# Kernel tuning notes

Hardware: AMD Instinct MI355X
Metric: run time of the kernel (lower is better)

The kernel has to match this reference:

```python
import jax, jax.numpy as jnp
import numpy as np

TOP_K = 2


def setup_inputs() -> dict:
    key = jax.random.key(0)
    k1, k2, k3, k4 = jax.random.split(key, 4)
    B, D, H, E = 16384, 1024, 1024, 8
    return {
        "x": jax.random.normal(k1, (B, D), dtype=jnp.float32),
        "Wv": jax.random.normal(k2, (E, D, H), dtype=jnp.float32),
        "Wg": jax.random.normal(k3, (E, D, H), dtype=jnp.float32),
        "gate_w": jax.random.normal(k4, (E, D), dtype=jnp.float32) * (1.0 / np.sqrt(D)),
        "gate_b": jnp.zeros((E,), dtype=jnp.float32),
    }


def reference(x, Wv, Wg, gate_w, gate_b):
    # Router: softmax over expert logits, then top-k selection.
    logits = x @ gate_w.T + gate_b                      # [B, E]
    probs = jax.nn.softmax(logits, axis=1)
    topk_scores, topk_idx = jax.lax.top_k(probs, TOP_K)  # [B, K]

    B, E = probs.shape
    # Scatter top-k scores into a dense [B, E] combine matrix (zeros elsewhere).
    combine = jnp.zeros((B, E), dtype=probs.dtype).at[
        jnp.arange(B)[:, None], topk_idx
    ].add(topk_scores)

    # Dense per-expert SwiGLU; combine matrix zeros out non-selected experts,
    # so the math matches the grouped-gemm top-k dispatch exactly.
    v = jnp.einsum("bd,edh->beh", x, Wv)                # [B, E, H]
    g = jnp.einsum("bd,edh->beh", x, Wg)                # [B, E, H]
    act = v * jax.nn.sigmoid(g)                         # SwiGLU-style gating
    return jnp.einsum("be,beh->bh", combine, act)       # weighted combine [B, H]
```

## Files before the change

kernel.cpp:

```cpp
#include <hip/hip_runtime.h>

#define D_DIM 1024
#define H_DIM 1024
#define E_NUM 8
#define BM 256
#define BN 256
#define BK 64
#define NT (D_DIM / BK)
#define CAP 5120
#define RT_TOK 32
#define RT_BLKS (16384 / RT_TOK)
#define TW_BLKS (16 * 16 * 2 * E_NUM)

typedef __attribute__((ext_vector_type(8))) _Float16 h8v;
typedef __attribute__((ext_vector_type(4))) float f4v;

__device__ __forceinline__ unsigned short f2h(float f) {
  union { _Float16 h; unsigned short u; } c;
  c.h = (_Float16)f;
  return c.u;
}

__device__ __forceinline__ void gl2lds16(const void* g, void* l) {
  __builtin_amdgcn_global_load_lds(
      (const __attribute__((address_space(1))) unsigned int*)g,
      (__attribute__((address_space(3))) unsigned int*)l, 16, 0, 0);
}

__device__ __forceinline__ unsigned ldsaddr(const void* p) {
  return (unsigned)(unsigned long long)(const __attribute__((address_space(3))) void*)p;
}

__global__ __launch_bounds__(256) void prep_kernel(
    const float4* __restrict__ x4, const float4* __restrict__ gw4,
    const float* __restrict__ gb, int* __restrict__ counts,
    int* __restrict__ bucket, float* __restrict__ scoreB,
    int* __restrict__ slotOf, ushort4* __restrict__ xh4,
    const float* __restrict__ Wv, const float* __restrict__ Wg,
    unsigned short* __restrict__ Wc) {
  __shared__ float4 gwS[E_NUM * 256];
  __shared__ float tile[64][65];
  __shared__ short eSelS[RT_TOK][2];
  __shared__ float sSelS[RT_TOK][2];
  __shared__ int lCnt[E_NUM], lBase[E_NUM];
  __shared__ unsigned char lOff[RT_TOK][2];
  int tid = threadIdx.x;
  int bid = blockIdx.x;

  if (bid >= RT_BLKS) {
    int fb = bid - RT_BLKS;
    int hx = fb & 15, dy = (fb >> 4) & 15, z = fb >> 8;
    const float* W = (z & 1) ? Wg : Wv;
    int mat = z & 1;
    int e = z >> 1;
    int h0 = hx * 64, d0 = dy * 64;
    const float* Wp = W + (size_t)e * D_DIM * H_DIM;
    unsigned short* Wcp = Wc + (size_t)e * (2 * H_DIM) * D_DIM;
#pragma unroll
    for (int j = 0; j < 4; j++) {
      int id = tid + 256 * j;
      int dd = id >> 4, hc = id & 15;
      float4 v = *(const float4*)(Wp + (size_t)(d0 + dd) * H_DIM + h0 + hc * 4);
      tile[dd][hc * 4 + 0] = v.x;
      tile[dd][hc * 4 + 1] = v.y;
      tile[dd][hc * 4 + 2] = v.z;
      tile[dd][hc * 4 + 3] = v.w;
    }
    __syncthreads();
#pragma unroll
    for (int j = 0; j < 2; j++) {
      int id = tid + 256 * j;
      int h_ = id >> 3, dc = id & 7;
      unsigned short tmp[8];
#pragma unroll
      for (int k = 0; k < 8; k++) tmp[k] = f2h(tile[dc * 8 + k][h_]);
      int hg = h0 + h_;
      int ng = ((hg >> 4) << 5) | (mat << 4) | (hg & 15);
      *(uint4*)(Wcp + (size_t)ng * D_DIM + d0 + dc * 8) = *(uint4*)tmp;
    }
    return;
  }

  for (int i = tid; i < E_NUM * 256; i += 256) gwS[i] = gw4[i];
  if (tid < E_NUM) lCnt[tid] = 0;
  __syncthreads();
  int wid = tid >> 6, lane = tid & 63;
  for (int rep = 0; rep < RT_TOK / 4; rep++) {
    int t = wid * (RT_TOK / 4) + rep;
    int b = bid * RT_TOK + t;
    float acc[E_NUM];
#pragma unroll
    for (int e = 0; e < E_NUM; e++) acc[e] = 0.0f;
#pragma unroll
    for (int i = 0; i < 4; i++) {
      float4 xv = x4[(size_t)b * 256 + i * 64 + lane];
      ushort4 o;
      o.x = f2h(xv.x); o.y = f2h(xv.y); o.z = f2h(xv.z); o.w = f2h(xv.w);
      xh4[(size_t)b * 256 + i * 64 + lane] = o;
#pragma unroll
      for (int e = 0; e < E_NUM; e++) {
        float4 w = gwS[e * 256 + i * 64 + lane];
        acc[e] += xv.x * w.x + xv.y * w.y + xv.z * w.z + xv.w * w.w;
      }
    }
#pragma unroll
    for (int e = 0; e < E_NUM; e++) {
#pragma unroll
      for (int off = 32; off > 0; off >>= 1) acc[e] += __shfl_down(acc[e], off);
    }
    if (lane == 0) {
      float l[E_NUM];
#pragma unroll
      for (int e = 0; e < E_NUM; e++) l[e] = acc[e] + gb[e];
      int i0 = 0;
#pragma unroll
      for (int e = 1; e < E_NUM; e++) if (l[e] > l[i0]) i0 = e;
      int i1 = (i0 == 0) ? 1 : 0;
#pragma unroll
      for (int e = 0; e < E_NUM; e++) if (e != i0 && l[e] > l[i1]) i1 = e;
      float mx = l[i0];
      float denom = 0.0f;
#pragma unroll
      for (int e = 0; e < E_NUM; e++) denom += __expf(l[e] - mx);
      eSelS[t][0] = (short)i0; sSelS[t][0] = 1.0f / denom;
      eSelS[t][1] = (short)i1; sSelS[t][1] = __expf(l[i1] - mx) / denom;
    }
  }
  __syncthreads();
  if (tid < RT_TOK) {
    lOff[tid][0] = (unsigned char)atomicAdd(&lCnt[eSelS[tid][0]], 1);
    lOff[tid][1] = (unsigned char)atomicAdd(&lCnt[eSelS[tid][1]], 1);
  }
  __syncthreads();
  if (tid < E_NUM) lBase[tid] = atomicAdd(&counts[tid * 32], lCnt[tid]);
  __syncthreads();
  if (tid < RT_TOK) {
    int b = bid * RT_TOK + tid;
#pragma unroll
    for (int j = 0; j < 2; j++) {
      int e = eSelS[tid][j];
      int pos = lBase[e] + lOff[tid][j];
      if (pos < CAP) {
        int slot = e * CAP + pos;
        bucket[slot] = b;
        scoreB[slot] = sSelS[tid][j];
        slotOf[b * 2 + j] = slot;
      }
    }
  }
}


#define DSR(dst, areg, IMM)                                                   \
  asm volatile("ds_read_b128 %0, %1 offset:%c2"                               \
               : "=v"(dst) : "v"(areg), "i"(IMM))

#define OFFS(CB, HI) ((CB) * 32768 + (HI) * 16384)

#define RD12_P0(CB) do {                                                      \
    DSR(bf[0][0], bB0, OFFS(CB, 0) + 0);                                      \
    DSR(bf[1][0], bB0, OFFS(CB, 0) + 2048);                                   \
    DSR(af[0][0], aA0, OFFS(CB, 0) + 0);                                      \
    DSR(af[1][0], aA0, OFFS(CB, 0) + 2048);                                   \
    DSR(af[2][0], aA0, OFFS(CB, 0) + 4096);                                   \
    DSR(af[3][0], aA0, OFFS(CB, 0) + 6144);                                   \
    DSR(bf[0][1], bB1, OFFS(CB, 0) + 0);                                      \
    DSR(bf[1][1], bB1, OFFS(CB, 0) + 2048);                                   \
    DSR(af[0][1], aA1, OFFS(CB, 0) + 0);                                      \
    DSR(af[1][1], aA1, OFFS(CB, 0) + 2048);                                   \
    DSR(af[2][1], aA1, OFFS(CB, 0) + 4096);                                   \
    DSR(af[3][1], aA1, OFFS(CB, 0) + 6144);                                   \
  } while (0)

#define RD8_A(CB, HI) do {                                                    \
    DSR(af[0][0], aA0, OFFS(CB, HI) + 0);                                     \
    DSR(af[1][0], aA0, OFFS(CB, HI) + 2048);                                  \
    DSR(af[2][0], aA0, OFFS(CB, HI) + 4096);                                  \
    DSR(af[3][0], aA0, OFFS(CB, HI) + 6144);                                  \
    DSR(af[0][1], aA1, OFFS(CB, HI) + 0);                                     \
    DSR(af[1][1], aA1, OFFS(CB, HI) + 2048);                                  \
    DSR(af[2][1], aA1, OFFS(CB, HI) + 4096);                                  \
    DSR(af[3][1], aA1, OFFS(CB, HI) + 6144);                                  \
  } while (0)

#define RD4_B(CB, HI) do {                                                    \
    DSR(bf[0][0], bB0, OFFS(CB, HI) + 0);                                     \
    DSR(bf[1][0], bB0, OFFS(CB, HI) + 2048);                                  \
    DSR(bf[0][1], bB1, OFFS(CB, HI) + 0);                                     \
    DSR(bf[1][1], bB1, OFFS(CB, HI) + 2048);                                  \
  } while (0)

#define MFMA_S(MO, NO, S)                                                     \
  {                                                                           \
    _Pragma("unroll") for (int m = 0; m < 4; m++) {                           \
      _Pragma("unroll") for (int n = 0; n < 2; n++) {                         \
        acc[(MO) + m][(NO) + n] = __builtin_amdgcn_mfma_f32_16x16x32_f16(     \
            af[m][S], bf[n][S], acc[(MO) + m][(NO) + n], 0, 0, 0);            \
      }                                                                       \
    }                                                                         \
  }

#define PH_BAR() __builtin_amdgcn_s_barrier()
#define LGKM(N) do {                                                          \
    asm volatile("s_waitcnt lgkmcnt(" #N ")" ::: "memory");                   \
    __builtin_amdgcn_sched_barrier(0);                                        \
  } while (0)
#define VMW(N) asm volatile("s_waitcnt vmcnt(" #N ")" ::: "memory")
#define PRIO1() __builtin_amdgcn_s_setprio(1)
#define PRIO0() __builtin_amdgcn_s_setprio(0)

#define TILE_N(CB) do {                                                       \
                           \
    RD12_P0(CB);                                                              \
    gl2lds16(pA[0], &As[(CB) ^ 1][0 * 4096 + dst0]);                          \
    gl2lds16(pA[1], &As[(CB) ^ 1][1 * 4096 + dst0]);                          \
    LGKM(6);  PRIO1(); MFMA_S(0, 0, 0); PRIO0();                              \
    LGKM(0);  PRIO1(); MFMA_S(0, 0, 1); PRIO0();                              \
    VMW(4); PH_BAR();                                                         \
                               \
    RD4_B(CB, 1);                                                             \
    gl2lds16(pB[0], &Bs[(CB) ^ 1][0 * 4096 + dst0]);                          \
    gl2lds16(pB[1], &Bs[(CB) ^ 1][1 * 4096 + dst0]);                          \
    LGKM(2);  PRIO1(); MFMA_S(0, 2, 0); PRIO0();                              \
    LGKM(0);  PRIO1(); MFMA_S(0, 2, 1); PRIO0();                              \
    VMW(4); PH_BAR();                                                         \
                   \
    RD8_A(CB, 1);                                                             \
    gl2lds16(pB[2], &Bs[(CB) ^ 1][2 * 4096 + dst0]);                          \
    gl2lds16(pB[3], &Bs[(CB) ^ 1][3 * 4096 + dst0]);                          \
    LGKM(4);  PRIO1(); MFMA_S(4, 2, 0); PRIO0();                              \
    LGKM(0);  PRIO1(); MFMA_S(4, 2, 1); PRIO0();                              \
                     \
    RD4_B(CB, 0);                                                             \
    gl2lds16(pA[2], &As[(CB) ^ 1][2 * 4096 + dst0]);                          \
    gl2lds16(pA[3], &As[(CB) ^ 1][3 * 4096 + dst0]);                          \
    LGKM(2);  PRIO1(); MFMA_S(4, 0, 0); PRIO0();                              \
    LGKM(0);  PRIO1(); MFMA_S(4, 0, 1); PRIO0();                              \
    VMW(4); PH_BAR();                                                         \
    _Pragma("unroll") for (int i = 0; i < 4; i++) { pA[i] += BK; pB[i] += BK; } \
  } while (0)

template <bool USE_PARTIAL>
__global__ __launch_bounds__(512, 2) void moe_gemm_kernel(
    const unsigned short* __restrict__ xh, const unsigned short* __restrict__ Wc,
    const int* __restrict__ counts, const int* __restrict__ bucket,
    const float* __restrict__ scoreB, _Float16* __restrict__ partial,
    float* __restrict__ out, int B) {
  int e = blockIdx.z;
  int cnt = counts[e * 32];
  int m0 = blockIdx.x * BM;
  if (m0 >= cnt) return;
  int n0 = blockIdx.y * BN;

  __shared__ unsigned short As[2][BM * BK];
  __shared__ unsigned short Bs[2][BN * BK];
  __shared__ int tokS[BM];
  __shared__ float scS[BM];

  int tid = threadIdx.x;
  if (tid < BM) {
    int gr = m0 + tid;
    bool vld = gr < cnt;
    tokS[tid] = vld ? bucket[e * CAP + gr] : 0;
    scS[tid] = vld ? scoreB[e * CAP + gr] : 0.0f;
  }
  __syncthreads();

  int wid = tid >> 6, lane = tid & 63;
  int wm = wid & 1, wn = wid >> 1;
  int quad = lane >> 4, lr = lane & 15;

  int rA = tid >> 3;
  int ksw = ((tid & 7) ^ (rA & 7)) * 8;
  const unsigned short* WcE = Wc + (size_t)e * (2 * H_DIM) * D_DIM;
  const unsigned short* pA[4];
  const unsigned short* pB[4];
#pragma unroll
  for (int i = 0; i < 4; i++) {
    pA[i] = xh + (size_t)tokS[i * 64 + rA] * D_DIM + ksw;
    pB[i] = WcE + (size_t)(n0 + i * 64 + rA) * D_DIM + ksw;
  }
  int dst0 = tid * 8;

  unsigned swz0 = (unsigned)(((0 * 4 + quad) ^ (lr & 7)) * 16);
  unsigned swz1 = (unsigned)(((1 * 4 + quad) ^ (lr & 7)) * 16);
  unsigned ldsA = ldsaddr(&As[0][0]);
  unsigned ldsB = ldsaddr(&Bs[0][0]);
  unsigned aA0 = ldsA + (unsigned)(wm * 8192 + lr * 128) + swz0;
  unsigned aA1 = ldsA + (unsigned)(wm * 8192 + lr * 128) + swz1;
  unsigned bB0 = ldsB + (unsigned)(wn * 4096 + lr * 128) + swz0;
  unsigned bB1 = ldsB + (unsigned)(wn * 4096 + lr * 128) + swz1;

  f4v acc[8][4];
#pragma unroll
  for (int m = 0; m < 8; m++)
#pragma unroll
    for (int n = 0; n < 4; n++) acc[m][n] = (f4v){0.f, 0.f, 0.f, 0.f};

  gl2lds16(pA[0], &As[0][0 * 4096 + dst0]);
  gl2lds16(pA[1], &As[0][1 * 4096 + dst0]);
  gl2lds16(pB[0], &Bs[0][0 * 4096 + dst0]);
  gl2lds16(pB[1], &Bs[0][1 * 4096 + dst0]);
  gl2lds16(pB[2], &Bs[0][2 * 4096 + dst0]);
  gl2lds16(pB[3], &Bs[0][3 * 4096 + dst0]);
  gl2lds16(pA[2], &As[0][2 * 4096 + dst0]);
  gl2lds16(pA[3], &As[0][3 * 4096 + dst0]);
#pragma unroll
  for (int i = 0; i < 4; i++) { pA[i] += BK; pB[i] += BK; }
  VMW(4);
  PH_BAR();

  h8v af[4][2], bf[2][2];

  for (int it = 0; it < 7; ++it) {
    TILE_N(0);
    TILE_N(1);
  }
  TILE_N(0);

  {
    RD12_P0(1);
    LGKM(6);  PRIO1(); MFMA_S(0, 0, 0); PRIO0();
    LGKM(0);  PRIO1(); MFMA_S(0, 0, 1); PRIO0();
    VMW(2); PH_BAR();
    RD4_B(1, 1);
    LGKM(2);  PRIO1(); MFMA_S(0, 2, 0); PRIO0();
    LGKM(0);  PRIO1(); MFMA_S(0, 2, 1); PRIO0();
    VMW(0); PH_BAR();
    RD8_A(1, 1);
    LGKM(4);  PRIO1(); MFMA_S(4, 2, 0); PRIO0();
    LGKM(0);  PRIO1(); MFMA_S(4, 2, 1); PRIO0();
    RD4_B(1, 0);
    LGKM(2);  PRIO1(); MFMA_S(4, 0, 0); PRIO0();
    LGKM(0);  PRIO1(); MFMA_S(4, 0, 1); PRIO0();
  }

  int hb = blockIdx.y * 128 + wn * 16 + lr;
#pragma unroll
  for (int m = 0; m < 8; m++) {
    int rb = ((m < 4) ? (wm * 64 + m * 16) : (128 + wm * 64 + (m - 4) * 16)) + quad * 4;
#pragma unroll
    for (int r = 0; r < 4; r++) {
      int rr = rb + r;
      float sc = scS[rr];
      if (USE_PARTIAL) {
        _Float16* pr = partial + (size_t)(e * CAP + m0 + rr) * H_DIM;
#pragma unroll
        for (int p = 0; p < 2; p++) {
          float v = acc[m][2 * p][r];
          float g = acc[m][2 * p + 1][r];
          pr[hb + p * 64] = (_Float16)(v * sc / (1.0f + __expf(-g)));
        }
      } else {
        int tok = tokS[rr];
#pragma unroll
        for (int p = 0; p < 2; p++) {
          float v = acc[m][2 * p][r];
          float g = acc[m][2 * p + 1][r];
          atomicAdd(&out[(size_t)tok * H_DIM + hb + p * 64],
                    v * sc / (1.0f + __expf(-g)));
        }
      }
    }
  }
}

__global__ __launch_bounds__(256) void gather_kernel(
    const _Float16* __restrict__ partial, const int* __restrict__ slotOf,
    float* __restrict__ out) {
  int b = blockIdx.x * 2 + (threadIdx.x >> 7);
  int t = threadIdx.x & 127;
  int s0 = slotOf[b * 2], s1 = slotOf[b * 2 + 1];
  if ((unsigned)s0 >= E_NUM * CAP) s0 = 0;
  if ((unsigned)s1 >= E_NUM * CAP) s1 = 0;
  h8v a = ((const h8v*)(partial + (size_t)s0 * H_DIM))[t];
  h8v c = ((const h8v*)(partial + (size_t)s1 * H_DIM))[t];
  float4 o0, o1;
  o0.x = (float)a[0] + (float)c[0];
  o0.y = (float)a[1] + (float)c[1];
  o0.z = (float)a[2] + (float)c[2];
  o0.w = (float)a[3] + (float)c[3];
  o1.x = (float)a[4] + (float)c[4];
  o1.y = (float)a[5] + (float)c[5];
  o1.z = (float)a[6] + (float)c[6];
  o1.w = (float)a[7] + (float)c[7];
  float4* op = (float4*)(out + (size_t)b * H_DIM);
  op[t * 2] = o0;
  op[t * 2 + 1] = o1;
}

extern "C" void kernel_launch(void* const* d_in, const int* in_sizes, int n_in,
                              void* d_out, int out_size, void* d_ws, size_t ws_size,
                              hipStream_t stream) {
  const float* x = (const float*)d_in[0];
  const float* Wv = (const float*)d_in[1];
  const float* Wg = (const float*)d_in[2];
  const float* gw = (const float*)d_in[3];
  const float* gb = (const float*)d_in[4];
  float* out = (float*)d_out;
  const int B = in_sizes[0] / D_DIM;

  char* ws = (char*)d_ws;
  unsigned short* xh = (unsigned short*)ws;
  size_t off = (size_t)B * D_DIM * 2;
  unsigned short* Wc = (unsigned short*)(ws + off);
  off += (size_t)E_NUM * (2 * H_DIM) * D_DIM * 2;
  int* counts = (int*)(ws + off);
  off += 4096;
  int* bucket = (int*)(ws + off);
  off += (size_t)E_NUM * CAP * 4;
  float* scoreB = (float*)(ws + off);
  off += (size_t)E_NUM * CAP * 4;
  int* slotOf = (int*)(ws + off);
  off += (size_t)B * 2 * 4;
  _Float16* partial = (_Float16*)(ws + off);
  size_t need = off + (size_t)E_NUM * CAP * H_DIM * 2;
  bool use_partial = ws_size >= need;

  hipMemsetAsync(counts, 0, 4096, stream);
  if (!use_partial) hipMemsetAsync(d_out, 0, (size_t)out_size * 4, stream);

  prep_kernel<<<RT_BLKS + TW_BLKS, 256, 0, stream>>>(
      (const float4*)x, (const float4*)gw, gb, counts, bucket, scoreB, slotOf,
      (ushort4*)xh, Wv, Wg, Wc);
  if (use_partial) {
    moe_gemm_kernel<true><<<dim3(CAP / BM, (2 * H_DIM) / BN, E_NUM), 512, 0, stream>>>(
        xh, Wc, counts, bucket, scoreB, partial, out, B);
    gather_kernel<<<B / 2, 256, 0, stream>>>(partial, slotOf, out);
  } else {
    moe_gemm_kernel<false><<<dim3(CAP / BM, (2 * H_DIM) / BN, E_NUM), 512, 0, stream>>>(
        xh, Wc, counts, bucket, scoreB, partial, out, B);
  }
}
```

Measured before the change: 353.9 us.

## Switch grouped GEMM to 32x32x16 MFMA with sliced LDS pipeline

Replaces the 16x16x32 MFMA tiling with 32x32x16 MFMA instructions, reorganizing the interleaved value/gate weight layout to 32-wide groups and rewriting LDS read addressing and swizzle accordingly. The main loop becomes a double-buffered slice pipeline alternating two register fragment sets, with a single barrier per K tile. The aim is fewer LDS reads per flop and higher MFMA throughput. The trade-off is a coarser global-load wait (vmcnt 0) that may expose load latency, and a different epilogue write pattern.

```diff
diff --git a/kernel.cpp b/kernel.cpp
--- a/kernel.cpp
+++ b/kernel.cpp
@@ -14,6 +14,7 @@
 
 typedef __attribute__((ext_vector_type(8))) _Float16 h8v;
 typedef __attribute__((ext_vector_type(4))) float f4v;
+typedef __attribute__((ext_vector_type(16))) float f16v;
 
 __device__ __forceinline__ unsigned short f2h(float f) {
   union { _Float16 h; unsigned short u; } c;
@@ -75,7 +76,7 @@
 #pragma unroll
       for (int k = 0; k < 8; k++) tmp[k] = f2h(tile[dc * 8 + k][h_]);
       int hg = h0 + h_;
-      int ng = ((hg >> 4) << 5) | (mat << 4) | (hg & 15);
+      int ng = ((hg >> 5) << 6) | (mat << 5) | (hg & 31);
       *(uint4*)(Wcp + (size_t)ng * D_DIM + d0 + dc * 8) = *(uint4*)tmp;
     }
     return;
@@ -155,50 +156,36 @@
   asm volatile("ds_read_b128 %0, %1 offset:%c2"                               \
                : "=v"(dst) : "v"(areg), "i"(IMM))
 
-#define OFFS(CB, HI) ((CB) * 32768 + (HI) * 16384)
-
-#define RD12_P0(CB) do {                                                      \
-    DSR(bf[0][0], bB0, OFFS(CB, 0) + 0);                                      \
-    DSR(bf[1][0], bB0, OFFS(CB, 0) + 2048);                                   \
-    DSR(af[0][0], aA0, OFFS(CB, 0) + 0);                                      \
-    DSR(af[1][0], aA0, OFFS(CB, 0) + 2048);                                   \
-    DSR(af[2][0], aA0, OFFS(CB, 0) + 4096);                                   \
-    DSR(af[3][0], aA0, OFFS(CB, 0) + 6144);                                   \
-    DSR(bf[0][1], bB1, OFFS(CB, 0) + 0);                                      \
-    DSR(bf[1][1], bB1, OFFS(CB, 0) + 2048);                                   \
-    DSR(af[0][1], aA1, OFFS(CB, 0) + 0);                                      \
-    DSR(af[1][1], aA1, OFFS(CB, 0) + 2048);                                   \
-    DSR(af[2][1], aA1, OFFS(CB, 0) + 4096);                                   \
-    DSR(af[3][1], aA1, OFFS(CB, 0) + 6144);                                   \
-  } while (0)
-
-#define RD8_A(CB, HI) do {                                                    \
-    DSR(af[0][0], aA0, OFFS(CB, HI) + 0);                                     \
-    DSR(af[1][0], aA0, OFFS(CB, HI) + 2048);                                  \
-    DSR(af[2][0], aA0, OFFS(CB, HI) + 4096);                                  \
-    DSR(af[3][0], aA0, OFFS(CB, HI) + 6144);                                  \
-    DSR(af[0][1], aA1, OFFS(CB, HI) + 0);                                     \
-    DSR(af[1][1], aA1, OFFS(CB, HI) + 2048);                                  \
-    DSR(af[2][1], aA1, OFFS(CB, HI) + 4096);                                  \
-    DSR(af[3][1], aA1, OFFS(CB, HI) + 6144);                                  \
-  } while (0)
-
-#define RD4_B(CB, HI) do {                                                    \
-    DSR(bf[0][0], bB0, OFFS(CB, HI) + 0);                                     \
-    DSR(bf[1][0], bB0, OFFS(CB, HI) + 2048);                                  \
-    DSR(bf[0][1], bB1, OFFS(CB, HI) + 0);                                     \
-    DSR(bf[1][1], bB1, OFFS(CB, HI) + 2048);                                  \
-  } while (0)
-
-#define MFMA_S(MO, NO, S)                                                     \
-  {                                                                           \
-    _Pragma("unroll") for (int m = 0; m < 4; m++) {                           \
-      _Pragma("unroll") for (int n = 0; n < 2; n++) {                         \
-        acc[(MO) + m][(NO) + n] = __builtin_amdgcn_mfma_f32_16x16x32_f16(     \
-            af[m][S], bf[n][S], acc[(MO) + m][(NO) + n], 0, 0, 0);            \
-      }                                                                       \
+#define RD_SLICE(S, CB, J) do {                                               \
+    DSR(af##S[0], aJ##J, (CB) * 32768 + 0);                                   \
+    DSR(af##S[1], aJ##J, (CB) * 32768 + 4096);                                \
+    DSR(af##S[2], aJ##J, (CB) * 32768 + 8192);                                \
+    DSR(af##S[3], aJ##J, (CB) * 32768 + 12288);                               \
+    DSR(bf##S[0], bJ##J, (CB) * 32768 + 0);                                   \
+    DSR(bf##S[1], bJ##J, (CB) * 32768 + 4096);                                \
+  } while (0)
+
+#define MFMA_SL(S) do {                                                       \
+    _Pragma("unroll") for (int mf = 0; mf < 4; mf++) {                        \
+      acc[mf][0] = __builtin_amdgcn_mfma_f32_32x32x16_f16(                    \
+          af##S[mf], bf##S[0], acc[mf][0], 0, 0, 0);                          \
+      acc[mf][1] = __builtin_amdgcn_mfma_f32_32x32x16_f16(                    \
+          af##S[mf], bf##S[1], acc[mf][1], 0, 0, 0);                          \
     }                                                                         \
-  }
+  } while (0)
+
+#define STG_A(NB) do {                                                        \
+    gl2lds16(pA[0], &As[NB][0 * 4096 + dst0]);                                \
+    gl2lds16(pA[1], &As[NB][1 * 4096 + dst0]);                                \
+    gl2lds16(pA[2], &As[NB][2 * 4096 + dst0]);                                \
+    gl2lds16(pA[3], &As[NB][3 * 4096 + dst0]);                                \
+  } while (0)
+#define STG_B(NB) do {                                                        \
+    gl2lds16(pB[0], &Bs[NB][0 * 4096 + dst0]);                                \
+    gl2lds16(pB[1], &Bs[NB][1 * 4096 + dst0]);                                \
+    gl2lds16(pB[2], &Bs[NB][2 * 4096 + dst0]);                                \
+    gl2lds16(pB[3], &Bs[NB][3 * 4096 + dst0]);                                \
+  } while (0)
 
 #define PH_BAR() __builtin_amdgcn_s_barrier()
 #define LGKM(N) do {                                                          \
@@ -209,35 +196,22 @@
 #define PRIO1() __builtin_amdgcn_s_setprio(1)
 #define PRIO0() __builtin_amdgcn_s_setprio(0)
 
-#define TILE_N(CB) do {                                                       \
-                           \
-    RD12_P0(CB);                                                              \
-    gl2lds16(pA[0], &As[(CB) ^ 1][0 * 4096 + dst0]);                          \
-    gl2lds16(pA[1], &As[(CB) ^ 1][1 * 4096 + dst0]);                          \
-    LGKM(6);  PRIO1(); MFMA_S(0, 0, 0); PRIO0();                              \
-    LGKM(0);  PRIO1(); MFMA_S(0, 0, 1); PRIO0();                              \
-    VMW(4); PH_BAR();                                                         \
-                               \
-    RD4_B(CB, 1);                                                             \
-    gl2lds16(pB[0], &Bs[(CB) ^ 1][0 * 4096 + dst0]);                          \
-    gl2lds16(pB[1], &Bs[(CB) ^ 1][1 * 4096 + dst0]);                          \
-    LGKM(2);  PRIO1(); MFMA_S(0, 2, 0); PRIO0();                              \
-    LGKM(0);  PRIO1(); MFMA_S(0, 2, 1); PRIO0();                              \
-    VMW(4); PH_BAR();                                                         \
-                   \
-    RD8_A(CB, 1);                                                             \
-    gl2lds16(pB[2], &Bs[(CB) ^ 1][2 * 4096 + dst0]);                          \
-    gl2lds16(pB[3], &Bs[(CB) ^ 1][3 * 4096 + dst0]);                          \
-    LGKM(4);  PRIO1(); MFMA_S(4, 2, 0); PRIO0();                              \
-    LGKM(0);  PRIO1(); MFMA_S(4, 2, 1); PRIO0();                              \
-                     \
-    RD4_B(CB, 0);                                                             \
-    gl2lds16(pA[2], &As[(CB) ^ 1][2 * 4096 + dst0]);                          \
-    gl2lds16(pA[3], &As[(CB) ^ 1][3 * 4096 + dst0]);                          \
-    LGKM(2);  PRIO1(); MFMA_S(4, 0, 0); PRIO0();                              \
-    LGKM(0);  PRIO1(); MFMA_S(4, 0, 1); PRIO0();                              \
-    VMW(4); PH_BAR();                                                         \
-    _Pragma("unroll") for (int i = 0; i < 4; i++) { pA[i] += BK; pB[i] += BK; } \
+#define TILE32(CB, STG) do {                                                  \
+    RD_SLICE(B, CB, 1);                                                       \
+    if (STG) STG_A((CB) ^ 1);                                                 \
+    LGKM(6); PRIO1(); MFMA_SL(A); PRIO0();                                    \
+    RD_SLICE(A, CB, 2);                                                       \
+    if (STG) STG_B((CB) ^ 1);                                                 \
+    LGKM(6); PRIO1(); MFMA_SL(B); PRIO0();                                    \
+    RD_SLICE(B, CB, 3);                                                       \
+    LGKM(6); PRIO1(); MFMA_SL(A); PRIO0();                                    \
+    LGKM(0);                                                                  \
+    if (STG) {                                                                \
+      VMW(0); PH_BAR();                                                       \
+      RD_SLICE(A, (CB) ^ 1, 0);                                               \
+      _Pragma("unroll") for (int i = 0; i < 4; i++) { pA[i] += BK; pB[i] += BK; } \
+    }                                                                         \
+    PRIO1(); MFMA_SL(B); PRIO0();                                             \
   } while (0)
 
 template <bool USE_PARTIAL>
@@ -268,7 +242,7 @@
 
   int wid = tid >> 6, lane = tid & 63;
   int wm = wid & 1, wn = wid >> 1;
-  int quad = lane >> 4, lr = lane & 15;
+  int l31 = lane & 31, hi = lane >> 5, l7 = lane & 7;
 
   int rA = tid >> 3;
   int ksw = ((tid & 7) ^ (rA & 7)) * 8;
@@ -282,84 +256,59 @@
   }
   int dst0 = tid * 8;
 
-  unsigned swz0 = (unsigned)(((0 * 4 + quad) ^ (lr & 7)) * 16);
-  unsigned swz1 = (unsigned)(((1 * 4 + quad) ^ (lr & 7)) * 16);
   unsigned ldsA = ldsaddr(&As[0][0]);
   unsigned ldsB = ldsaddr(&Bs[0][0]);
-  unsigned aA0 = ldsA + (unsigned)(wm * 8192 + lr * 128) + swz0;
-  unsigned aA1 = ldsA + (unsigned)(wm * 8192 + lr * 128) + swz1;
-  unsigned bB0 = ldsB + (unsigned)(wn * 4096 + lr * 128) + swz0;
-  unsigned bB1 = ldsB + (unsigned)(wn * 4096 + lr * 128) + swz1;
-
-  f4v acc[8][4];
-#pragma unroll
-  for (int m = 0; m < 8; m++)
-#pragma unroll
-    for (int n = 0; n < 4; n++) acc[m][n] = (f4v){0.f, 0.f, 0.f, 0.f};
-
-  gl2lds16(pA[0], &As[0][0 * 4096 + dst0]);
-  gl2lds16(pA[1], &As[0][1 * 4096 + dst0]);
-  gl2lds16(pB[0], &Bs[0][0 * 4096 + dst0]);
-  gl2lds16(pB[1], &Bs[0][1 * 4096 + dst0]);
-  gl2lds16(pB[2], &Bs[0][2 * 4096 + dst0]);
-  gl2lds16(pB[3], &Bs[0][3 * 4096 + dst0]);
-  gl2lds16(pA[2], &As[0][2 * 4096 + dst0]);
-  gl2lds16(pA[3], &As[0][3 * 4096 + dst0]);
+  unsigned aB = ldsA + (unsigned)(wm * 16384 + l31 * 128);
+  unsigned bB = ldsB + (unsigned)(wn * 8192 + l31 * 128);
+  unsigned aJ0 = aB + (unsigned)(((0 + hi) ^ l7) * 16);
+  unsigned aJ1 = aB + (unsigned)(((2 + hi) ^ l7) * 16);
+  unsigned aJ2 = aB + (unsigned)(((4 + hi) ^ l7) * 16);
+  unsigned aJ3 = aB + (unsigned)(((6 + hi) ^ l7) * 16);
+  unsigned bJ0 = bB + (unsigned)(((0 + hi) ^ l7) * 16);
+  unsigned bJ1 = bB + (unsigned)(((2 + hi) ^ l7) * 16);
+  unsigned bJ2 = bB + (unsigned)(((4 + hi) ^ l7) * 16);
+  unsigned bJ3 = bB + (unsigned)(((6 + hi) ^ l7) * 16);
+
+  f16v acc[4][2];
+#pragma unroll
+  for (int m = 0; m < 4; m++)
+#pragma unroll
+    for (int n = 0; n < 2; n++)
+#pragma unroll
+      for (int r = 0; r < 16; r++) acc[m][n][r] = 0.0f;
+
+  STG_A(0);
+  STG_B(0);
 #pragma unroll
   for (int i = 0; i < 4; i++) { pA[i] += BK; pB[i] += BK; }
-  VMW(4);
+  VMW(0);
   PH_BAR();
 
-  h8v af[4][2], bf[2][2];
+  h8v afA[4], bfA[2], afB[4], bfB[2];
+  RD_SLICE(A, 0, 0);
 
   for (int it = 0; it < 7; ++it) {
-    TILE_N(0);
-    TILE_N(1);
-  }
-  TILE_N(0);
-
-  {
-    RD12_P0(1);
-    LGKM(6);  PRIO1(); MFMA_S(0, 0, 0); PRIO0();
-    LGKM(0);  PRIO1(); MFMA_S(0, 0, 1); PRIO0();
-    VMW(2); PH_BAR();
-    RD4_B(1, 1);
-    LGKM(2);  PRIO1(); MFMA_S(0, 2, 0); PRIO0();
-    LGKM(0);  PRIO1(); MFMA_S(0, 2, 1); PRIO0();
-    VMW(0); PH_BAR();
-    RD8_A(1, 1);
-    LGKM(4);  PRIO1(); MFMA_S(4, 2, 0); PRIO0();
-    LGKM(0);  PRIO1(); MFMA_S(4, 2, 1); PRIO0();
-    RD4_B(1, 0);
-    LGKM(2);  PRIO1(); MFMA_S(4, 0, 0); PRIO0();
-    LGKM(0);  PRIO1(); MFMA_S(4, 0, 1); PRIO0();
-  }
-
-  int hb = blockIdx.y * 128 + wn * 16 + lr;
-#pragma unroll
-  for (int m = 0; m < 8; m++) {
-    int rb = ((m < 4) ? (wm * 64 + m * 16) : (128 + wm * 64 + (m - 4) * 16)) + quad * 4;
-#pragma unroll
-    for (int r = 0; r < 4; r++) {
-      int rr = rb + r;
-      float sc = scS[rr];
+    TILE32(0, 1);
+    TILE32(1, 1);
+  }
+  TILE32(0, 1);
+  TILE32(1, 0);
+  LGKM(0);
+
+  int hb = blockIdx.y * 128 + wn * 32 + l31;
+#pragma unroll
+  for (int mf = 0; mf < 4; mf++) {
+#pragma unroll
+    for (int r = 0; r < 16; r++) {
+      int row = wm * 128 + mf * 32 + (r & 3) + 8 * (r >> 2) + 4 * hi;
+      float sc = scS[row];
+      float v = acc[mf][0][r];
+      float g = acc[mf][1][r];
+      float o = v * sc / (1.0f + __expf(-g));
       if (USE_PARTIAL) {
-        _Float16* pr = partial + (size_t)(e * CAP + m0 + rr) * H_DIM;
-#pragma unroll
-        for (int p = 0; p < 2; p++) {
-          float v = acc[m][2 * p][r];
-          float g = acc[m][2 * p + 1][r];
-          pr[hb + p * 64] = (_Float16)(v * sc / (1.0f + __expf(-g)));
-        }
+        partial[(size_t)(e * CAP + m0 + row) * H_DIM + hb] = (_Float16)o;
       } else {
-        int tok = tokS[rr];
-#pragma unroll
-        for (int p = 0; p < 2; p++) {
-          float v = acc[m][2 * p][r];
-          float g = acc[m][2 * p + 1][r];
-          atomicAdd(&out[(size_t)tok * H_DIM + hb + p * 64],
-                    v * sc / (1.0f + __expf(-g)));
-        }
+        atomicAdd(&out[(size_t)tokS[row] * H_DIM + hb], o);
       }
     }
   }
```

Result: slower. 374.0 us (+5.7%).
